# Performance work log

Hardware: AMD Instinct MI355X
Metric: run time of the kernel (lower is better)

## Reference

```python
import jax, jax.numpy as jnp
import numpy as np

B = 256          # graphs per batch
NR = 268         # ROIs (nodes) per graph
N = B * NR       # total nodes
IC, OC = 256, 64 # in/out channels
NC = 7           # communities
DEG = 32
E = N * DEG      # total edges
K = int(NR * 0.8)  # 214 nodes kept per graph (floor, as torch .long())
LN_EPS = 1e-5


def setup_inputs() -> dict:
    key = jax.random.key(0)
    ks = jax.random.split(key, 10)
    x = jax.random.normal(ks[0], (N, IC), jnp.float32)
    # within-graph random edges: local src/dst in [0, NR) plus per-graph offset
    src = jax.random.randint(ks[1], (E,), 0, NR, dtype=jnp.int32)
    dst = jax.random.randint(ks[2], (E,), 0, NR, dtype=jnp.int32)
    off = jnp.repeat(jnp.arange(B, dtype=jnp.int32) * NR, NR * DEG)
    edge_index = jnp.stack([src + off, dst + off])  # (2, E)
    edge_attr = jax.random.uniform(ks[3], (E, 1), jnp.float32)
    batch = jnp.repeat(jnp.arange(B, dtype=jnp.int32), NR)
    xav = lambda k, shp: jax.random.normal(k, shp, jnp.float32) * np.float32(
        np.sqrt(2.0 / (shp[-2] + shp[-1])))
    return {
        "x": x, "edge_index": edge_index, "edge_attr": edge_attr, "batch": batch,
        "basis_kernels": xav(ks[4], (NC, IC, OC)),
        "roi_community": xav(ks[5], (NR, NC)),
        "ew_w": xav(ks[6], (1, OC)), "ew_b": jnp.zeros((OC,), jnp.float32),
        "conv_bias": jnp.zeros((OC,), jnp.float32),
        "ln_gamma": jnp.ones((OC,), jnp.float32), "ln_beta": jnp.zeros((OC,), jnp.float32),
        "att_w1": xav(ks[7], (OC, OC)), "att_b1": jnp.zeros((OC,), jnp.float32),
        "att_w2": xav(ks[8], (OC, 1)), "att_b2": jnp.zeros((1,), jnp.float32),
    }


def reference(x, edge_index, edge_attr, batch, basis_kernels, roi_community,
              ew_w, ew_b, conv_bias, ln_gamma, ln_beta,
              att_w1, att_b1, att_w2, att_b2):
    n = x.shape[0]
    loops = jnp.arange(n, dtype=edge_index.dtype)
    ei = jnp.concatenate([edge_index, jnp.stack([loops, loops])], axis=1)  # add self loops
    ea = jnp.concatenate([edge_attr, jnp.ones((n, 1), x.dtype)], axis=0)   # fill_value=1.0

    # ROI-aware kernels: per-node mixture of basis kernels
    cw = jax.nn.softmax(roi_community, axis=-1)            # (NR, NC)
    roi_k = jnp.einsum('rc,cio->rio', cw, basis_kernels)   # (NR, IC, OC)
    node_ids = loops % NR
    node_k = roi_k[node_ids]                               # (N, IC, OC) gather
    xt = jnp.einsum('ni,nio->no', x, node_k)               # per-node bmm

    # edge-gated message passing, scatter-add aggregation
    gate = jax.nn.sigmoid(ea @ ew_w + ew_b)                # (E+N, OC)
    msg = xt[ei[0]] * gate
    out = jax.ops.segment_sum(msg, ei[1], num_segments=n) + conv_bias

    out = jax.nn.elu(out)
    mu = jnp.mean(out, axis=-1, keepdims=True)
    var = jnp.mean(jnp.square(out - mu), axis=-1, keepdims=True)
    h = (out - mu) * jax.lax.rsqrt(var + LN_EPS) * ln_gamma + ln_beta
    # dropout: eval mode (identity)

    # R-pool: per-graph top-k (all graphs have NR contiguous nodes)
    scores = (jnp.tanh(h @ att_w1 + att_b1) @ att_w2 + att_b2).squeeze(-1)  # (N,)
    top_v, top_i = jax.lax.top_k(scores.reshape(B, NR), K)                  # (B, K)
    perm = (top_i.astype(jnp.int32) + jnp.arange(B, dtype=jnp.int32)[:, None] * NR).reshape(-1)
    x_pooled = h[perm] * jax.nn.sigmoid(top_v.reshape(-1))[:, None]
    batch_pooled = batch[perm]
    return x_pooled, batch_pooled, scores, perm
```

## Files before the change

kernel.cpp:

```cpp
#include <hip/hip_runtime.h>
#include <cstdint>
#include <cstddef>

#define NR   268
#define NB   256
#define NN   (NR*NB)
#define IC   256
#define OC   64
#define DEG  32
#define EPG  (NR*DEG)
#define NE   (NN*DEG)
#define KK   214

#define XP_OFF 0
#define BP_OFF 3506176
#define SC_OFF 3560960
#define PM_OFF 3629568

#define WS_XT   4390912
#define WS_META 8781824
#define WS_ROWS 13369344

#define PPG   4480
#define ZROW  (NR*OC)

typedef float v2f __attribute__((ext_vector_type(2)));

__device__ __forceinline__ v2f pkfma(v2f a, v2f b, v2f c) {
    v2f d;
    asm("v_pk_fma_f32 %0, %1, %2, %3" : "=v"(d) : "v"(a), "v"(b), "v"(c));
    return d;
}

#define NREP2 8
#define GS3 130
#define FRONT_LDS 64512
__global__ __launch_bounds__(512) void k_front(const float* __restrict__ rc,
                                               const float* __restrict__ basis,
                                               const float* __restrict__ x,
                                               float* __restrict__ xt,
                                               const int* __restrict__ ei,
                                               const float* __restrict__ ea,
                                               float* __restrict__ meta,
                                               unsigned int* __restrict__ rows) {
    extern __shared__ __align__(16) unsigned char dynsm[];
    int bid = blockIdx.x;
    int tid = threadIdx.x;
    bool csr_role = (bid < 768) && (bid % 3 == 1);

    if (csr_role) {
        int g = bid / 3;
        unsigned int* cnt = (unsigned int*)dynsm;
        unsigned int* tot = cnt + NREP2*NR;
        unsigned int* prs = tot + NR;
        unsigned int* pkb = prs + NR;
        float* daA = (float*)(pkb + PPG);
        float* daB = daA + PPG;
        int wid = tid >> 6;
        for (int i = tid; i < NREP2*NR; i += 512) cnt[i] = 0u;
        for (int i = tid; i < PPG; i += 512) pkb[i] = 0u;
        __syncthreads();
        int ebase = g * EPG;
        for (int e = tid; e < EPG; e += 512) {
            int ld = ei[NE + ebase + e] - g * NR;
            atomicAdd(&cnt[wid*NR + ld], 1u);
        }
        __syncthreads();
        for (int r = tid; r < NR; r += 512) {
            unsigned t = 0;
#pragma unroll
            for (int s = 0; s < NREP2; ++s) t += cnt[s*NR + r];
            tot[r] = t;
        }
        __syncthreads();
        if (tid < 64) {
            unsigned run = 0;
            for (int base = 0; base < NR; base += 64) {
                int idx = base + tid;
                unsigned v = (idx < NR) ? ((tot[idx] + 1u) >> 1) : 0u;
                unsigned orig = v;
#pragma unroll
                for (int s = 1; s < 64; s <<= 1) {
                    int t = __shfl_up((int)v, (unsigned)s, 64);
                    if (tid >= s) v += (unsigned)t;
                }
                if (idx < NR) prs[idx] = run + v - orig;
                run += (unsigned)__shfl((int)v, 63, 64);
            }
        }
        __syncthreads();
        for (int r = tid; r < NR; r += 512) {
            unsigned base = 0;
#pragma unroll
            for (int s = 0; s < NREP2; ++s) {
                unsigned t = cnt[s*NR + r]; cnt[s*NR + r] = base; base += t;
            }
        }
        __syncthreads();
        unsigned lastPairs = (tot[NR-1] + 1u) >> 1;
        for (int i = tid; i < NR + 1; i += 512)
            rows[(size_t)g * (NR + 1) + i] =
                (i < NR) ? prs[i] : (prs[NR-1] + lastPairs);
        for (int e = tid; e < EPG; e += 512) {
            int src = ei[ebase + e] - g * NR;
            int ld  = ei[NE + ebase + e] - g * NR;
            float a = ea[ebase + e];
            unsigned rank = atomicAdd(&cnt[wid*NR + ld], 1u);
            unsigned p = prs[ld] + (rank >> 1), sl = rank & 1u;
            atomicOr(&pkb[p], ((unsigned)src) << (16u * sl));
            if (sl) daB[p] = a - 0.5f; else daA[p] = a - 0.5f;
        }
        for (int r = tid; r < NR; r += 512) {
            if (tot[r] & 1u) {
                unsigned p = prs[r] + (tot[r] >> 1);
                atomicOr(&pkb[p], 268u << 16);
                daB[p] = 0.f;
            }
        }
        __syncthreads();
        unsigned nPairs = prs[NR-1] + lastPairs;
        float4* __restrict__ mg = (float4*)(meta + (size_t)g * PPG * 4);
        for (unsigned i = tid; i < nPairs; i += 512) {
            unsigned pk = pkb[i];
            float4 f;
            f.x = __int_as_float((int)(pk & 0xFFFFu) * OC);
            f.y = __int_as_float((int)(pk >> 16) * OC);
            f.z = daA[i];
            f.w = daB[i];
            mg[i] = f;
        }
        return;
    }

    int idx = bid - ((bid < 768) ? (bid + 2) / 3 : 256);
    int r = idx % NR;
    int half = idx / NR;
    float* sXT = (float*)dynsm;
    float* sW  = sXT + 32 * GS3;

    int lane = tid & 63;
    int wu = __builtin_amdgcn_readfirstlane(tid >> 6);
    int g0 = lane * 2;
    int o0 = wu * 8;

    float cw[7];
    {
        float m = -1e30f;
#pragma unroll
        for (int j = 0; j < 7; ++j) { cw[j] = rc[r*7 + j]; m = fmaxf(m, cw[j]); }
        float s = 0.f;
#pragma unroll
        for (int j = 0; j < 7; ++j) { cw[j] = expf(cw[j] - m); s += cw[j]; }
        float inv = 1.f / s;
#pragma unroll
        for (int j = 0; j < 7; ++j) cw[j] *= inv;
    }

    int quad = tid & 7, grp = tid >> 3;
    const float* __restrict__ xrowA =
        x + ((size_t)(half*128 + grp) * NR + r) * IC + quad*4;
    const float* __restrict__ xrowB = xrowA + (size_t)64 * NR * IC;

    float acc[2][8];
#pragma unroll
    for (int i = 0; i < 2; ++i)
#pragma unroll
        for (int j = 0; j < 8; ++j) acc[i][j] = 0.f;

    for (int kt = 0; kt < IC; kt += 32) {
        __syncthreads();
        {
            float4 xa = *(const float4*)(xrowA + kt);
            float4 xb = *(const float4*)(xrowB + kt);
            sXT[(quad*4+0)*GS3 + grp] = xa.x;
            sXT[(quad*4+1)*GS3 + grp] = xa.y;
            sXT[(quad*4+2)*GS3 + grp] = xa.z;
            sXT[(quad*4+3)*GS3 + grp] = xa.w;
            sXT[(quad*4+0)*GS3 + 64 + grp] = xb.x;
            sXT[(quad*4+1)*GS3 + 64 + grp] = xb.y;
            sXT[(quad*4+2)*GS3 + 64 + grp] = xb.z;
            sXT[(quad*4+3)*GS3 + 64 + grp] = xb.w;
            int e0 = kt*OC + tid*4;
            float4 w4 = make_float4(0.f, 0.f, 0.f, 0.f);
#pragma unroll
            for (int j = 0; j < 7; ++j) {
                float4 bv = *(const float4*)(basis + (size_t)j*IC*OC + e0);
                w4.x = fmaf(cw[j], bv.x, w4.x);
                w4.y = fmaf(cw[j], bv.y, w4.y);
                w4.z = fmaf(cw[j], bv.z, w4.z);
                w4.w = fmaf(cw[j], bv.w, w4.w);
            }
            *(float4*)(sW + tid*4) = w4;
        }
        __syncthreads();

#pragma unroll 8
        for (int k = 0; k < 32; ++k) {
            float2 xa = *(const float2*)&sXT[k*GS3 + g0];
            float4 wa = *(const float4*)&sW[k*OC + o0];
            float4 wb = *(const float4*)&sW[k*OC + o0 + 4];
            acc[0][0] = fmaf(xa.x, wa.x, acc[0][0]);
            acc[1][0] = fmaf(xa.y, wa.x, acc[1][0]);
            acc[0][1] = fmaf(xa.x, wa.y, acc[0][1]);
            acc[1][1] = fmaf(xa.y, wa.y, acc[1][1]);
            acc[0][2] = fmaf(xa.x, wa.z, acc[0][2]);
            acc[1][2] = fmaf(xa.y, wa.z, acc[1][2]);
            acc[0][3] = fmaf(xa.x, wa.w, acc[0][3]);
            acc[1][3] = fmaf(xa.y, wa.w, acc[1][3]);
            acc[0][4] = fmaf(xa.x, wb.x, acc[0][4]);
            acc[1][4] = fmaf(xa.y, wb.x, acc[1][4]);
            acc[0][5] = fmaf(xa.x, wb.y, acc[0][5]);
            acc[1][5] = fmaf(xa.y, wb.y, acc[1][5]);
            acc[0][6] = fmaf(xa.x, wb.z, acc[0][6]);
            acc[1][6] = fmaf(xa.y, wb.z, acc[1][6]);
            acc[0][7] = fmaf(xa.x, wb.w, acc[0][7]);
            acc[1][7] = fmaf(xa.y, wb.w, acc[1][7]);
        }
    }

#pragma unroll
    for (int i = 0; i < 2; ++i) {
        int g = half*128 + g0 + i;
        float* p = xt + ((size_t)g * NR + r) * OC + o0;
        float4 a; a.x = acc[i][0]; a.y = acc[i][1]; a.z = acc[i][2]; a.w = acc[i][3];
        float4 b; b.x = acc[i][4]; b.y = acc[i][5]; b.z = acc[i][6]; b.w = acc[i][7];
        *(float4*)p = a;
        *(float4*)(p + 4) = b;
    }
}

__global__ __launch_bounds__(1024, 4) void k_fused(
    const float* __restrict__ xt,
    const float4* __restrict__ meta,
    const unsigned int* __restrict__ rows,
    const float* __restrict__ ew_w, const float* __restrict__ ew_b,
    const float* __restrict__ conv_bias,
    const float* __restrict__ ln_g, const float* __restrict__ ln_b,
    const float* __restrict__ w1, const float* __restrict__ b1,
    const float* __restrict__ w2, const float* __restrict__ b2,
    float* __restrict__ out)
{
    extern __shared__ float smem[];
    float* xts = smem;
    float* hls = smem + (NR*OC + 64);
    __shared__ float rowbuf[16][OC];
    __shared__ float scl[NR];
    __shared__ int ord[KK];

    int g = blockIdx.x;
    int tid = threadIdx.x;
    int o = tid & 63, w = tid >> 6;

    {
        const float4* s4 = (const float4*)(xt + (size_t)g * NR * OC);
        float4* d4 = (float4*)xts;
        for (int i = tid; i < NR*OC/4; i += 1024) d4[i] = s4[i];
        if (tid < 16) d4[NR*OC/4 + tid] = make_float4(0.f, 0.f, 0.f, 0.f);
    }

    float wo = ew_w[o], bo = ew_b[o], cb = conv_bias[o];
    float lng = ln_g[o], lnb = ln_b[o];
    float w2o = w2[o], b1o = b1[o], b2s = b2[0];
    float sgself = 1.f / (1.f + expf(-(wo + bo)));

    float z0 = fmaf(0.5f, wo, bo);
    float sg0 = 1.f / (1.f + expf(-z0));
    float u  = sg0 * (1.f - sg0);
    float d2 = u * (1.f - 2.f*sg0);
    float d3 = u * (1.f - 6.f*u);
    float d4c = d2 * (1.f - 12.f*u);
    float k1 = u * wo;
    float k2 = d2 * wo*wo * 0.5f;
    float k3 = d3 * wo*wo*wo * (1.f/6.f);
    float k4 = d4c * wo*wo*wo*wo * (1.f/24.f);
    v2f kd4 = {k4, k4}, kd3 = {k3, k3}, kd2 = {k2, k2}, kd1 = {k1, k1};
    v2f sdv = {sg0, sg0};

    #define LOADW(j) \
        v2f wcA##j = { w1[(4*j+0)*OC+o], w1[(4*j+1)*OC+o] }; \
        v2f wcB##j = { w1[(4*j+2)*OC+o], w1[(4*j+3)*OC+o] };
    LOADW(0)  LOADW(1)  LOADW(2)  LOADW(3)
    LOADW(4)  LOADW(5)  LOADW(6)  LOADW(7)
    LOADW(8)  LOADW(9)  LOADW(10) LOADW(11)
    LOADW(12) LOADW(13) LOADW(14) LOADW(15)
    #undef LOADW

    const float4* __restrict__ gm = meta + (size_t)g * PPG;
    const unsigned int* __restrict__ gr = rows + (size_t)g * (NR + 1);
    const float* __restrict__ xo = xts + o;
    __syncthreads();

    #define PAIR(mp, acc) { \
        v2f xv; \
        xv.x = xo[__float_as_int((mp).x)]; \
        xv.y = xo[__float_as_int((mp).y)]; \
        v2f dv = { (mp).z, (mp).w }; \
        v2f t = pkfma(kd4, dv, kd3); \
        t = pkfma(t, dv, kd2); \
        t = pkfma(t, dv, kd1); \
        t = pkfma(t, dv, sdv); \
        acc = pkfma(xv, t, acc); }

    for (int r = w; r < NR; r += 16) {
        unsigned js = __builtin_amdgcn_readfirstlane(gr[r]);
        unsigned je = __builtin_amdgcn_readfirstlane(gr[r + 1]);
        v2f acc; acc.x = xts[r*OC + o] * sgself; acc.y = 0.f;
        unsigned j = js;
        for (; j + 8 <= je; j += 8) {
            float4 m0 = gm[j],   m1 = gm[j+1], m2 = gm[j+2], m3 = gm[j+3];
            float4 m4 = gm[j+4], m5 = gm[j+5], m6 = gm[j+6], m7 = gm[j+7];
            PAIR(m0, acc) PAIR(m1, acc) PAIR(m2, acc) PAIR(m3, acc)
            PAIR(m4, acc) PAIR(m5, acc) PAIR(m6, acc) PAIR(m7, acc)
        }
        if (j + 4 <= je) {
            float4 m0 = gm[j], m1 = gm[j+1], m2 = gm[j+2], m3 = gm[j+3];
            PAIR(m0, acc) PAIR(m1, acc) PAIR(m2, acc) PAIR(m3, acc)
            j += 4;
        }
        for (; j < je; ++j) {
            float4 m0 = gm[j];
            PAIR(m0, acc)
        }
        float accs = acc.x + acc.y + cb;
        float v = accs > 0.f ? accs : expm1f(accs);
        float s1 = v;
#pragma unroll
        for (int m = 1; m < 64; m <<= 1) s1 += __shfl_xor(s1, m, 64);
        float mu = s1 * (1.f/64.f);
        float d = v - mu;
        float s2 = d * d;
#pragma unroll
        for (int m = 1; m < 64; m <<= 1) s2 += __shfl_xor(s2, m, 64);
        float rsd = rsqrtf(s2 * (1.f/64.f) + 1e-5f);
        float h = fmaf(d * rsd, lng, lnb);
        hls[r*OC + o] = h;
        rowbuf[w][o] = h;
        {
            const float* hr = rowbuf[w];
            v2f tA = { b1o, 0.f }, tB = { 0.f, 0.f };
            #define STEP(j) { float4 h4 = *(const float4*)(hr + 4*j); \
                v2f hl = { h4.x, h4.y }, hh = { h4.z, h4.w }; \
                tA = pkfma(hl, wcA##j, tA); tB = pkfma(hh, wcB##j, tB); }
            STEP(0)  STEP(1)  STEP(2)  STEP(3)
            STEP(4)  STEP(5)  STEP(6)  STEP(7)
            STEP(8)  STEP(9)  STEP(10) STEP(11)
            STEP(12) STEP(13) STEP(14) STEP(15)
            #undef STEP
            float t = (tA.x + tA.y) + (tB.x + tB.y);
            float a2 = fminf(fmaxf(2.f * t, -80.f), 80.f);
            float y = expf(a2);
            float th = (y - 1.f) / (y + 1.f);
            float p = th * w2o;
#pragma unroll
            for (int m = 1; m < 64; m <<= 1) p += __shfl_xor(p, m, 64);
            if (o == 0) {
                float sc = p + b2s;
                scl[r] = sc;
                out[SC_OFF + (size_t)g * NR + r] = sc;
            }
        }
    }
    #undef PAIR
    __syncthreads();

    if (tid < NR) {
        float sr = scl[tid];
        int rank = 0;
        for (int jj = 0; jj < NR; ++jj) {
            float sj = scl[jj];
            rank += (sj > sr) || (sj == sr && jj < tid);
        }
        if (rank < KK) ord[rank] = tid;
    }
    __syncthreads();

    for (int k = w; k < KK; k += 16) {
        int r = ord[k];
        float v = scl[r];
        float gate = 1.f / (1.f + expf(-v));
        float hvv = hls[r*OC + o];
        out[XP_OFF + ((size_t)g*KK + k)*64 + o] = hvv * gate;
        if (o == 0) {
            out[BP_OFF + (size_t)g*KK + k] = (float)g;
            out[PM_OFF + (size_t)g*KK + k] = (float)(g*NR + r);
        }
    }
}

extern "C" void kernel_launch(void* const* d_in, const int* in_sizes, int n_in,
                              void* d_out, int out_size, void* d_ws, size_t ws_size,
                              hipStream_t stream) {
    const float* x     = (const float*)d_in[0];
    const int*   ei    = (const int*)d_in[1];
    const float* ea    = (const float*)d_in[2];
    const float* basis = (const float*)d_in[4];
    const float* rc    = (const float*)d_in[5];
    const float* ew_w  = (const float*)d_in[6];
    const float* ew_b  = (const float*)d_in[7];
    const float* cbias = (const float*)d_in[8];
    const float* ln_g  = (const float*)d_in[9];
    const float* ln_b  = (const float*)d_in[10];
    const float* w1    = (const float*)d_in[11];
    const float* b1    = (const float*)d_in[12];
    const float* w2    = (const float*)d_in[13];
    const float* b2    = (const float*)d_in[14];
    float* out = (float*)d_out;

    float* wsf = (float*)d_ws;
    float* xtb  = wsf + WS_XT;
    float* metaF = wsf + WS_META;
    unsigned int* rows = (unsigned int*)(wsf + WS_ROWS);

    size_t fused_lds = (size_t)(NR*OC + 64 + NR*OC) * sizeof(float);

    k_front<<<dim3(792), dim3(512), FRONT_LDS, stream>>>(rc, basis, x, xtb,
                                                         ei, ea, metaF, rows);
    k_fused<<<dim3(NB),  dim3(1024), fused_lds, stream>>>(
                                                  xtb, (const float4*)metaF, rows,
                                                  ew_w, ew_b, cbias, ln_g, ln_b,
                                                  w1, b1, w2, b2, out);
}
```

Before: 273.3 us.

## Move per-graph CSR build into fused aggregation kernel, keep edge records in LDS

The per-graph CSR construction (counting, scan, packing edge records) moves out of the front kernel's dedicated blocks and into the start of the fused aggregation kernel. Edge records now live in LDS instead of a global meta buffer, and normalized h rows are written to a global workspace instead of a second LDS copy to make room. This removes the global meta/rows round-trip and the mixed-role front kernel. In exchange, the fused kernel does the serial CSR build before aggregation (256 blocks only), and the final pooled gather reads h from global memory.

```diff
diff --git a/kernel.cpp b/kernel.cpp
--- a/kernel.cpp
+++ b/kernel.cpp
@@ -17,9 +17,8 @@
 #define SC_OFF 3560960
 #define PM_OFF 3629568
 
+#define WS_HB   0
 #define WS_XT   4390912
-#define WS_META 8781824
-#define WS_ROWS 13369344
 
 #define PPG   4480
 #define ZROW  (NR*OC)
@@ -32,112 +31,18 @@
     return d;
 }
 
-#define NREP2 8
 #define GS3 130
-#define FRONT_LDS 64512
-__global__ __launch_bounds__(512) void k_front(const float* __restrict__ rc,
-                                               const float* __restrict__ basis,
-                                               const float* __restrict__ x,
-                                               float* __restrict__ xt,
-                                               const int* __restrict__ ei,
-                                               const float* __restrict__ ea,
-                                               float* __restrict__ meta,
-                                               unsigned int* __restrict__ rows) {
-    extern __shared__ __align__(16) unsigned char dynsm[];
+__global__ __launch_bounds__(512) void k_xt(const float* __restrict__ rc,
+                                            const float* __restrict__ basis,
+                                            const float* __restrict__ x,
+                                            float* __restrict__ xt) {
+    __shared__ __align__(16) float sXT[32 * GS3];
+    __shared__ __align__(16) float sW[32 * OC];
+
     int bid = blockIdx.x;
+    int r = bid % NR;
+    int half = bid / NR;
     int tid = threadIdx.x;
-    bool csr_role = (bid < 768) && (bid % 3 == 1);
-
-    if (csr_role) {
-        int g = bid / 3;
-        unsigned int* cnt = (unsigned int*)dynsm;
-        unsigned int* tot = cnt + NREP2*NR;
-        unsigned int* prs = tot + NR;
-        unsigned int* pkb = prs + NR;
-        float* daA = (float*)(pkb + PPG);
-        float* daB = daA + PPG;
-        int wid = tid >> 6;
-        for (int i = tid; i < NREP2*NR; i += 512) cnt[i] = 0u;
-        for (int i = tid; i < PPG; i += 512) pkb[i] = 0u;
-        __syncthreads();
-        int ebase = g * EPG;
-        for (int e = tid; e < EPG; e += 512) {
-            int ld = ei[NE + ebase + e] - g * NR;
-            atomicAdd(&cnt[wid*NR + ld], 1u);
-        }
-        __syncthreads();
-        for (int r = tid; r < NR; r += 512) {
-            unsigned t = 0;
-#pragma unroll
-            for (int s = 0; s < NREP2; ++s) t += cnt[s*NR + r];
-            tot[r] = t;
-        }
-        __syncthreads();
-        if (tid < 64) {
-            unsigned run = 0;
-            for (int base = 0; base < NR; base += 64) {
-                int idx = base + tid;
-                unsigned v = (idx < NR) ? ((tot[idx] + 1u) >> 1) : 0u;
-                unsigned orig = v;
-#pragma unroll
-                for (int s = 1; s < 64; s <<= 1) {
-                    int t = __shfl_up((int)v, (unsigned)s, 64);
-                    if (tid >= s) v += (unsigned)t;
-                }
-                if (idx < NR) prs[idx] = run + v - orig;
-                run += (unsigned)__shfl((int)v, 63, 64);
-            }
-        }
-        __syncthreads();
-        for (int r = tid; r < NR; r += 512) {
-            unsigned base = 0;
-#pragma unroll
-            for (int s = 0; s < NREP2; ++s) {
-                unsigned t = cnt[s*NR + r]; cnt[s*NR + r] = base; base += t;
-            }
-        }
-        __syncthreads();
-        unsigned lastPairs = (tot[NR-1] + 1u) >> 1;
-        for (int i = tid; i < NR + 1; i += 512)
-            rows[(size_t)g * (NR + 1) + i] =
-                (i < NR) ? prs[i] : (prs[NR-1] + lastPairs);
-        for (int e = tid; e < EPG; e += 512) {
-            int src = ei[ebase + e] - g * NR;
-            int ld  = ei[NE + ebase + e] - g * NR;
-            float a = ea[ebase + e];
-            unsigned rank = atomicAdd(&cnt[wid*NR + ld], 1u);
-            unsigned p = prs[ld] + (rank >> 1), sl = rank & 1u;
-            atomicOr(&pkb[p], ((unsigned)src) << (16u * sl));
-            if (sl) daB[p] = a - 0.5f; else daA[p] = a - 0.5f;
-        }
-        for (int r = tid; r < NR; r += 512) {
-            if (tot[r] & 1u) {
-                unsigned p = prs[r] + (tot[r] >> 1);
-                atomicOr(&pkb[p], 268u << 16);
-                daB[p] = 0.f;
-            }
-        }
-        __syncthreads();
-        unsigned nPairs = prs[NR-1] + lastPairs;
-        float4* __restrict__ mg = (float4*)(meta + (size_t)g * PPG * 4);
-        for (unsigned i = tid; i < nPairs; i += 512) {
-            unsigned pk = pkb[i];
-            float4 f;
-            f.x = __int_as_float((int)(pk & 0xFFFFu) * OC);
-            f.y = __int_as_float((int)(pk >> 16) * OC);
-            f.z = daA[i];
-            f.w = daB[i];
-            mg[i] = f;
-        }
-        return;
-    }
-
-    int idx = bid - ((bid < 768) ? (bid + 2) / 3 : 256);
-    int r = idx % NR;
-    int half = idx / NR;
-    float* sXT = (float*)dynsm;
-    float* sW  = sXT + 32 * GS3;
-
     int lane = tid & 63;
     int wu = __builtin_amdgcn_readfirstlane(tid >> 6);
     int g0 = lane * 2;
@@ -229,10 +134,11 @@
     }
 }
 
-__global__ __launch_bounds__(1024, 4) void k_fused(
+#define NREPF 8
+__global__ __launch_bounds__(1024, 4) void k_fuse(
     const float* __restrict__ xt,
-    const float4* __restrict__ meta,
-    const unsigned int* __restrict__ rows,
+    const int* __restrict__ ei, const float* __restrict__ ea,
+    float* __restrict__ hbw,
     const float* __restrict__ ew_w, const float* __restrict__ ew_b,
     const float* __restrict__ conv_bias,
     const float* __restrict__ ln_g, const float* __restrict__ ln_b,
@@ -240,9 +146,11 @@
     const float* __restrict__ w2, const float* __restrict__ b2,
     float* __restrict__ out)
 {
-    extern __shared__ float smem[];
-    float* xts = smem;
-    float* hls = smem + (NR*OC + 64);
+    extern __shared__ __align__(16) unsigned char dynsm[];
+    float4* rec = (float4*)dynsm;
+    float* xts = (float*)(dynsm + (size_t)PPG * 16);
+    __shared__ unsigned int cnt[NREPF][NR];
+    __shared__ unsigned int rowse[NR + 1];
     __shared__ float rowbuf[16][OC];
     __shared__ float scl[NR];
     __shared__ int ord[KK];
@@ -250,12 +158,73 @@
     int g = blockIdx.x;
     int tid = threadIdx.x;
     int o = tid & 63, w = tid >> 6;
+    unsigned int* tot = (unsigned int*)scl;
 
     {
         const float4* s4 = (const float4*)(xt + (size_t)g * NR * OC);
         float4* d4 = (float4*)xts;
         for (int i = tid; i < NR*OC/4; i += 1024) d4[i] = s4[i];
         if (tid < 16) d4[NR*OC/4 + tid] = make_float4(0.f, 0.f, 0.f, 0.f);
+    }
+
+    for (int i = tid; i < NREPF*NR; i += 1024) ((unsigned*)cnt)[i] = 0u;
+    __syncthreads();
+    int wid = tid >> 7;
+    int ebase = g * EPG;
+    for (int e = tid; e < EPG; e += 1024) {
+        int ld = ei[NE + ebase + e] - g * NR;
+        atomicAdd(&cnt[wid][ld], 1u);
+    }
+    __syncthreads();
+    for (int r = tid; r < NR; r += 1024) {
+        unsigned t = 0;
+#pragma unroll
+        for (int s = 0; s < NREPF; ++s) t += cnt[s][r];
+        tot[r] = t;
+    }
+    __syncthreads();
+    if (tid < 64) {
+        unsigned run = 0;
+        for (int base = 0; base < NR; base += 64) {
+            int idx = base + tid;
+            unsigned v = (idx < NR) ? ((tot[idx] + 1u) >> 1) : 0u;
+            unsigned orig = v;
+#pragma unroll
+            for (int s = 1; s < 64; s <<= 1) {
+                int t = __shfl_up((int)v, (unsigned)s, 64);
+                if (tid >= s) v += (unsigned)t;
+            }
+            if (idx < NR) rowse[idx] = run + v - orig;
+            run += (unsigned)__shfl((int)v, 63, 64);
+        }
+        if (tid == 0) rowse[NR] = run;
+    }
+    __syncthreads();
+    for (int r = tid; r < NR; r += 1024) {
+        unsigned base = 0;
+#pragma unroll
+        for (int s = 0; s < NREPF; ++s) {
+            unsigned t = cnt[s][r]; cnt[s][r] = base; base += t;
+        }
+    }
+    __syncthreads();
+    for (int e = tid; e < EPG; e += 1024) {
+        int src = ei[ebase + e] - g * NR;
+        int ld  = ei[NE + ebase + e] - g * NR;
+        float a = ea[ebase + e];
+        unsigned rank = atomicAdd(&cnt[wid][ld], 1u);
+        unsigned p = rowse[ld] + (rank >> 1), sl = rank & 1u;
+        float* rp = (float*)&rec[p];
+        rp[sl]     = __int_as_float(src * OC);
+        rp[2 + sl] = a - 0.5f;
+    }
+    for (int r = tid; r < NR; r += 1024) {
+        if (tot[r] & 1u) {
+            unsigned p = rowse[r] + (tot[r] >> 1);
+            float* rp = (float*)&rec[p];
+            rp[1] = __int_as_float(ZROW);
+            rp[3] = 0.f;
+        }
     }
 
     float wo = ew_w[o], bo = ew_b[o], cb = conv_bias[o];
@@ -285,8 +254,7 @@
     LOADW(12) LOADW(13) LOADW(14) LOADW(15)
     #undef LOADW
 
-    const float4* __restrict__ gm = meta + (size_t)g * PPG;
-    const unsigned int* __restrict__ gr = rows + (size_t)g * (NR + 1);
+    const float4* __restrict__ gm = rec;
     const float* __restrict__ xo = xts + o;
     __syncthreads();
 
@@ -302,20 +270,13 @@
         acc = pkfma(xv, t, acc); }
 
     for (int r = w; r < NR; r += 16) {
-        unsigned js = __builtin_amdgcn_readfirstlane(gr[r]);
-        unsigned je = __builtin_amdgcn_readfirstlane(gr[r + 1]);
+        unsigned js = __builtin_amdgcn_readfirstlane(rowse[r]);
+        unsigned je = __builtin_amdgcn_readfirstlane(rowse[r + 1]);
         v2f acc; acc.x = xts[r*OC + o] * sgself; acc.y = 0.f;
         unsigned j = js;
-        for (; j + 8 <= je; j += 8) {
-            float4 m0 = gm[j],   m1 = gm[j+1], m2 = gm[j+2], m3 = gm[j+3];
-            float4 m4 = gm[j+4], m5 = gm[j+5], m6 = gm[j+6], m7 = gm[j+7];
-            PAIR(m0, acc) PAIR(m1, acc) PAIR(m2, acc) PAIR(m3, acc)
-            PAIR(m4, acc) PAIR(m5, acc) PAIR(m6, acc) PAIR(m7, acc)
-        }
-        if (j + 4 <= je) {
+        for (; j + 4 <= je; j += 4) {
             float4 m0 = gm[j], m1 = gm[j+1], m2 = gm[j+2], m3 = gm[j+3];
             PAIR(m0, acc) PAIR(m1, acc) PAIR(m2, acc) PAIR(m3, acc)
-            j += 4;
         }
         for (; j < je; ++j) {
             float4 m0 = gm[j];
@@ -333,7 +294,7 @@
         for (int m = 1; m < 64; m <<= 1) s2 += __shfl_xor(s2, m, 64);
         float rsd = rsqrtf(s2 * (1.f/64.f) + 1e-5f);
         float h = fmaf(d * rsd, lng, lnb);
-        hls[r*OC + o] = h;
+        hbw[((size_t)g * NR + r)*OC + o] = h;
         rowbuf[w][o] = h;
         {
             const float* hr = rowbuf[w];
@@ -378,7 +339,7 @@
         int r = ord[k];
         float v = scl[r];
         float gate = 1.f / (1.f + expf(-v));
-        float hvv = hls[r*OC + o];
+        float hvv = hbw[((size_t)g * NR + r)*OC + o];
         out[XP_OFF + ((size_t)g*KK + k)*64 + o] = hvv * gate;
         if (o == 0) {
             out[BP_OFF + (size_t)g*KK + k] = (float)g;
@@ -407,16 +368,14 @@
     float* out = (float*)d_out;
 
     float* wsf = (float*)d_ws;
-    float* xtb  = wsf + WS_XT;
-    float* metaF = wsf + WS_META;
-    unsigned int* rows = (unsigned int*)(wsf + WS_ROWS);
-
-    size_t fused_lds = (size_t)(NR*OC + 64 + NR*OC) * sizeof(float);
-
-    k_front<<<dim3(792), dim3(512), FRONT_LDS, stream>>>(rc, basis, x, xtb,
-                                                         ei, ea, metaF, rows);
-    k_fused<<<dim3(NB),  dim3(1024), fused_lds, stream>>>(
-                                                  xtb, (const float4*)metaF, rows,
+    float* hbw = wsf + WS_HB;
+    float* xtb = wsf + WS_XT;
+
+    size_t fuse_lds = (size_t)PPG * 16 + (size_t)(NR*OC + 64) * 4;
+
+    k_xt  <<<dim3(NR*2), dim3(512), 0, stream>>>(rc, basis, x, xtb);
+    k_fuse<<<dim3(NB),   dim3(1024), fuse_lds, stream>>>(
+                                                  xtb, ei, ea, hbw,
                                                   ew_w, ew_b, cbias, ln_g, ln_b,
                                                   w1, b1, w2, b2, out);
 }
```

New measurement: 272.3 us. Within noise of the previous version (-0.4%).

## Prefetch next K-tile in front GEMM and interleave two rows in aggregation

Applied to the files above, without the earlier changes.

In the front kernel, the x and basis loads for the next 32-wide K tile are issued right after the barrier, so they overlap with the current tile's FMA loop. Launch bounds now request 4 blocks per CU. In the fused kernel, each wave processes two rows (r and r+16) together, alternating their edge gathers to expose more independent memory loads. This raises register pressure, and the min-blocks hint may force spills.

```diff
diff --git a/kernel.cpp b/kernel.cpp
--- a/kernel.cpp
+++ b/kernel.cpp
@@ -35,14 +35,14 @@
 #define NREP2 8
 #define GS3 130
 #define FRONT_LDS 64512
-__global__ __launch_bounds__(512) void k_front(const float* __restrict__ rc,
-                                               const float* __restrict__ basis,
-                                               const float* __restrict__ x,
-                                               float* __restrict__ xt,
-                                               const int* __restrict__ ei,
-                                               const float* __restrict__ ea,
-                                               float* __restrict__ meta,
-                                               unsigned int* __restrict__ rows) {
+__global__ __launch_bounds__(512, 4) void k_front(const float* __restrict__ rc,
+                                                  const float* __restrict__ basis,
+                                                  const float* __restrict__ x,
+                                                  float* __restrict__ xt,
+                                                  const int* __restrict__ ei,
+                                                  const float* __restrict__ ea,
+                                                  float* __restrict__ meta,
+                                                  unsigned int* __restrict__ rows) {
     extern __shared__ __align__(16) unsigned char dynsm[];
     int bid = blockIdx.x;
     int tid = threadIdx.x;
@@ -167,54 +167,73 @@
 #pragma unroll
         for (int j = 0; j < 8; ++j) acc[i][j] = 0.f;
 
+    float4 xa = *(const float4*)(xrowA);
+    float4 xb = *(const float4*)(xrowB);
+    float4 bv0, bv1, bv2, bv3, bv4, bv5, bv6;
+    {
+        int e0 = tid*4;
+        bv0 = *(const float4*)(basis + (size_t)0*IC*OC + e0);
+        bv1 = *(const float4*)(basis + (size_t)1*IC*OC + e0);
+        bv2 = *(const float4*)(basis + (size_t)2*IC*OC + e0);
+        bv3 = *(const float4*)(basis + (size_t)3*IC*OC + e0);
+        bv4 = *(const float4*)(basis + (size_t)4*IC*OC + e0);
+        bv5 = *(const float4*)(basis + (size_t)5*IC*OC + e0);
+        bv6 = *(const float4*)(basis + (size_t)6*IC*OC + e0);
+    }
+
     for (int kt = 0; kt < IC; kt += 32) {
-        __syncthreads();
-        {
-            float4 xa = *(const float4*)(xrowA + kt);
-            float4 xb = *(const float4*)(xrowB + kt);
-            sXT[(quad*4+0)*GS3 + grp] = xa.x;
-            sXT[(quad*4+1)*GS3 + grp] = xa.y;
-            sXT[(quad*4+2)*GS3 + grp] = xa.z;
-            sXT[(quad*4+3)*GS3 + grp] = xa.w;
-            sXT[(quad*4+0)*GS3 + 64 + grp] = xb.x;
-            sXT[(quad*4+1)*GS3 + 64 + grp] = xb.y;
-            sXT[(quad*4+2)*GS3 + 64 + grp] = xb.z;
-            sXT[(quad*4+3)*GS3 + 64 + grp] = xb.w;
-            int e0 = kt*OC + tid*4;
-            float4 w4 = make_float4(0.f, 0.f, 0.f, 0.f);
-#pragma unroll
-            for (int j = 0; j < 7; ++j) {
-                float4 bv = *(const float4*)(basis + (size_t)j*IC*OC + e0);
-                w4.x = fmaf(cw[j], bv.x, w4.x);
-                w4.y = fmaf(cw[j], bv.y, w4.y);
-                w4.z = fmaf(cw[j], bv.z, w4.z);
-                w4.w = fmaf(cw[j], bv.w, w4.w);
-            }
-            *(float4*)(sW + tid*4) = w4;
-        }
-        __syncthreads();
+        float4 w4 = make_float4(0.f, 0.f, 0.f, 0.f);
+        #define WACC(J) { w4.x = fmaf(cw[J], bv##J.x, w4.x); \
+                          w4.y = fmaf(cw[J], bv##J.y, w4.y); \
+                          w4.z = fmaf(cw[J], bv##J.z, w4.z); \
+                          w4.w = fmaf(cw[J], bv##J.w, w4.w); }
+        WACC(0) WACC(1) WACC(2) WACC(3) WACC(4) WACC(5) WACC(6)
+        #undef WACC
+        __syncthreads();
+        sXT[(quad*4+0)*GS3 + grp] = xa.x;
+        sXT[(quad*4+1)*GS3 + grp] = xa.y;
+        sXT[(quad*4+2)*GS3 + grp] = xa.z;
+        sXT[(quad*4+3)*GS3 + grp] = xa.w;
+        sXT[(quad*4+0)*GS3 + 64 + grp] = xb.x;
+        sXT[(quad*4+1)*GS3 + 64 + grp] = xb.y;
+        sXT[(quad*4+2)*GS3 + 64 + grp] = xb.z;
+        sXT[(quad*4+3)*GS3 + 64 + grp] = xb.w;
+        *(float4*)(sW + tid*4) = w4;
+        __syncthreads();
+        if (kt + 32 < IC) {
+            xa = *(const float4*)(xrowA + kt + 32);
+            xb = *(const float4*)(xrowB + kt + 32);
+            int e0 = (kt + 32)*OC + tid*4;
+            bv0 = *(const float4*)(basis + (size_t)0*IC*OC + e0);
+            bv1 = *(const float4*)(basis + (size_t)1*IC*OC + e0);
+            bv2 = *(const float4*)(basis + (size_t)2*IC*OC + e0);
+            bv3 = *(const float4*)(basis + (size_t)3*IC*OC + e0);
+            bv4 = *(const float4*)(basis + (size_t)4*IC*OC + e0);
+            bv5 = *(const float4*)(basis + (size_t)5*IC*OC + e0);
+            bv6 = *(const float4*)(basis + (size_t)6*IC*OC + e0);
+        }
 
 #pragma unroll 8
         for (int k = 0; k < 32; ++k) {
-            float2 xa = *(const float2*)&sXT[k*GS3 + g0];
+            float2 xv = *(const float2*)&sXT[k*GS3 + g0];
             float4 wa = *(const float4*)&sW[k*OC + o0];
             float4 wb = *(const float4*)&sW[k*OC + o0 + 4];
-            acc[0][0] = fmaf(xa.x, wa.x, acc[0][0]);
-            acc[1][0] = fmaf(xa.y, wa.x, acc[1][0]);
-            acc[0][1] = fmaf(xa.x, wa.y, acc[0][1]);
-            acc[1][1] = fmaf(xa.y, wa.y, acc[1][1]);
-            acc[0][2] = fmaf(xa.x, wa.z, acc[0][2]);
-            acc[1][2] = fmaf(xa.y, wa.z, acc[1][2]);
-            acc[0][3] = fmaf(xa.x, wa.w, acc[0][3]);
-            acc[1][3] = fmaf(xa.y, wa.w, acc[1][3]);
-            acc[0][4] = fmaf(xa.x, wb.x, acc[0][4]);
-            acc[1][4] = fmaf(xa.y, wb.x, acc[1][4]);
-            acc[0][5] = fmaf(xa.x, wb.y, acc[0][5]);
-            acc[1][5] = fmaf(xa.y, wb.y, acc[1][5]);
-            acc[0][6] = fmaf(xa.x, wb.z, acc[0][6]);
-            acc[1][6] = fmaf(xa.y, wb.z, acc[1][6]);
-            acc[0][7] = fmaf(xa.x, wb.w, acc[0][7]);
-            acc[1][7] = fmaf(xa.y, wb.w, acc[1][7]);
+            acc[0][0] = fmaf(xv.x, wa.x, acc[0][0]);
+            acc[1][0] = fmaf(xv.y, wa.x, acc[1][0]);
+            acc[0][1] = fmaf(xv.x, wa.y, acc[0][1]);
+            acc[1][1] = fmaf(xv.y, wa.y, acc[1][1]);
+            acc[0][2] = fmaf(xv.x, wa.z, acc[0][2]);
+            acc[1][2] = fmaf(xv.y, wa.z, acc[1][2]);
+            acc[0][3] = fmaf(xv.x, wa.w, acc[0][3]);
+            acc[1][3] = fmaf(xv.y, wa.w, acc[1][3]);
+            acc[0][4] = fmaf(xv.x, wb.x, acc[0][4]);
+            acc[1][4] = fmaf(xv.y, wb.x, acc[1][4]);
+            acc[0][5] = fmaf(xv.x, wb.y, acc[0][5]);
+            acc[1][5] = fmaf(xv.y, wb.y, acc[1][5]);
+            acc[0][6] = fmaf(xv.x, wb.z, acc[0][6]);
+            acc[1][6] = fmaf(xv.y, wb.z, acc[1][6]);
+            acc[0][7] = fmaf(xv.x, wb.w, acc[0][7]);
+            acc[1][7] = fmaf(xv.y, wb.w, acc[1][7]);
         }
     }
 
@@ -301,26 +320,7 @@
         t = pkfma(t, dv, sdv); \
         acc = pkfma(xv, t, acc); }
 
-    for (int r = w; r < NR; r += 16) {
-        unsigned js = __builtin_amdgcn_readfirstlane(gr[r]);
-        unsigned je = __builtin_amdgcn_readfirstlane(gr[r + 1]);
-        v2f acc; acc.x = xts[r*OC + o] * sgself; acc.y = 0.f;
-        unsigned j = js;
-        for (; j + 8 <= je; j += 8) {
-            float4 m0 = gm[j],   m1 = gm[j+1], m2 = gm[j+2], m3 = gm[j+3];
-            float4 m4 = gm[j+4], m5 = gm[j+5], m6 = gm[j+6], m7 = gm[j+7];
-            PAIR(m0, acc) PAIR(m1, acc) PAIR(m2, acc) PAIR(m3, acc)
-            PAIR(m4, acc) PAIR(m5, acc) PAIR(m6, acc) PAIR(m7, acc)
-        }
-        if (j + 4 <= je) {
-            float4 m0 = gm[j], m1 = gm[j+1], m2 = gm[j+2], m3 = gm[j+3];
-            PAIR(m0, acc) PAIR(m1, acc) PAIR(m2, acc) PAIR(m3, acc)
-            j += 4;
-        }
-        for (; j < je; ++j) {
-            float4 m0 = gm[j];
-            PAIR(m0, acc)
-        }
+    auto finish = [&](int r, v2f acc) {
         float accs = acc.x + acc.y + cb;
         float v = accs > 0.f ? accs : expm1f(accs);
         float s1 = v;
@@ -335,30 +335,65 @@
         float h = fmaf(d * rsd, lng, lnb);
         hls[r*OC + o] = h;
         rowbuf[w][o] = h;
-        {
-            const float* hr = rowbuf[w];
-            v2f tA = { b1o, 0.f }, tB = { 0.f, 0.f };
-            #define STEP(j) { float4 h4 = *(const float4*)(hr + 4*j); \
-                v2f hl = { h4.x, h4.y }, hh = { h4.z, h4.w }; \
-                tA = pkfma(hl, wcA##j, tA); tB = pkfma(hh, wcB##j, tB); }
-            STEP(0)  STEP(1)  STEP(2)  STEP(3)
-            STEP(4)  STEP(5)  STEP(6)  STEP(7)
-            STEP(8)  STEP(9)  STEP(10) STEP(11)
-            STEP(12) STEP(13) STEP(14) STEP(15)
-            #undef STEP
-            float t = (tA.x + tA.y) + (tB.x + tB.y);
-            float a2 = fminf(fmaxf(2.f * t, -80.f), 80.f);
-            float y = expf(a2);
-            float th = (y - 1.f) / (y + 1.f);
-            float p = th * w2o;
-#pragma unroll
-            for (int m = 1; m < 64; m <<= 1) p += __shfl_xor(p, m, 64);
-            if (o == 0) {
-                float sc = p + b2s;
-                scl[r] = sc;
-                out[SC_OFF + (size_t)g * NR + r] = sc;
-            }
-        }
+        const float* hr = rowbuf[w];
+        v2f tA = { b1o, 0.f }, tB = { 0.f, 0.f };
+        #define STEP(j) { float4 h4 = *(const float4*)(hr + 4*j); \
+            v2f hl = { h4.x, h4.y }, hh = { h4.z, h4.w }; \
+            tA = pkfma(hl, wcA##j, tA); tB = pkfma(hh, wcB##j, tB); }
+        STEP(0)  STEP(1)  STEP(2)  STEP(3)
+        STEP(4)  STEP(5)  STEP(6)  STEP(7)
+        STEP(8)  STEP(9)  STEP(10) STEP(11)
+        STEP(12) STEP(13) STEP(14) STEP(15)
+        #undef STEP
+        float t = (tA.x + tA.y) + (tB.x + tB.y);
+        float a2 = fminf(fmaxf(2.f * t, -80.f), 80.f);
+        float y = expf(a2);
+        float th = (y - 1.f) / (y + 1.f);
+        float p = th * w2o;
+#pragma unroll
+        for (int m = 1; m < 64; m <<= 1) p += __shfl_xor(p, m, 64);
+        if (o == 0) {
+            float sc = p + b2s;
+            scl[r] = sc;
+            out[SC_OFF + (size_t)g * NR + r] = sc;
+        }
+    };
+
+    for (int i0 = 0; i0 < NR; i0 += 32) {
+        int r1 = i0 + w;
+        if (r1 >= NR) continue;
+        int r2 = r1 + 16;
+        bool has2 = (r2 < NR);
+        unsigned js1 = __builtin_amdgcn_readfirstlane(gr[r1]);
+        unsigned je1 = __builtin_amdgcn_readfirstlane(gr[r1 + 1]);
+        unsigned j2 = 0, je2 = 0;
+        v2f acc1; acc1.x = xts[r1*OC + o] * sgself; acc1.y = 0.f;
+        v2f acc2; acc2.x = 0.f; acc2.y = 0.f;
+        if (has2) {
+            j2  = __builtin_amdgcn_readfirstlane(gr[r2]);
+            je2 = __builtin_amdgcn_readfirstlane(gr[r2 + 1]);
+            acc2.x = xts[r2*OC + o] * sgself;
+        }
+        unsigned j1 = js1;
+        while (j1 + 4 <= je1 && j2 + 4 <= je2) {
+            float4 a0 = gm[j1], a1 = gm[j1+1], a2 = gm[j1+2], a3 = gm[j1+3];
+            float4 b0 = gm[j2], b1 = gm[j2+1], b2 = gm[j2+2], b3 = gm[j2+3];
+            PAIR(a0, acc1) PAIR(a1, acc1) PAIR(a2, acc1) PAIR(a3, acc1)
+            PAIR(b0, acc2) PAIR(b1, acc2) PAIR(b2, acc2) PAIR(b3, acc2)
+            j1 += 4; j2 += 4;
+        }
+        for (; j1 + 4 <= je1; j1 += 4) {
+            float4 a0 = gm[j1], a1 = gm[j1+1], a2 = gm[j1+2], a3 = gm[j1+3];
+            PAIR(a0, acc1) PAIR(a1, acc1) PAIR(a2, acc1) PAIR(a3, acc1)
+        }
+        for (; j1 < je1; ++j1) { float4 a0 = gm[j1]; PAIR(a0, acc1) }
+        for (; j2 + 4 <= je2; j2 += 4) {
+            float4 b0 = gm[j2], b1 = gm[j2+1], b2 = gm[j2+2], b3 = gm[j2+3];
+            PAIR(b0, acc2) PAIR(b1, acc2) PAIR(b2, acc2) PAIR(b3, acc2)
+        }
+        for (; j2 < je2; ++j2) { float4 b0 = gm[j2]; PAIR(b0, acc2) }
+        finish(r1, acc1);
+        if (has2) finish(r2, acc2);
     }
     #undef PAIR
     __syncthreads();
```

New measurement: 274.6 us. No clear change (+0.5%).
